# Performance work log

Hardware: AMD Instinct MI355X
Metric: run time of the kernel (lower is better)

Reference implementation:

```python
import jax, jax.numpy as jnp
import numpy as np
import math

B, H, W, C = 8, 32, 32, 512
NUM_HEAD_CHANNELS = 64
NUM_HEADS = C // NUM_HEAD_CHANNELS  # 8
HEAD_DIM = C // NUM_HEADS            # 64
NUM_GROUPS = max(1, C // 16)         # 32
EPS = 1e-6  # flax GroupNorm default epsilon


def setup_inputs() -> dict:
    key = jax.random.key(0)
    ks = jax.random.split(key, 7)
    s = lambda fan: 1.0 / math.sqrt(fan)
    return {
        "x": jax.random.normal(ks[0], (B, H, W, C), jnp.float32),
        "gn_scale": jnp.ones((C,), jnp.float32),
        "gn_bias": jnp.zeros((C,), jnp.float32),
        "w_qkv": jax.random.normal(ks[1], (C, 3 * C), jnp.float32) * s(C),
        "b_qkv": jnp.zeros((3 * C,), jnp.float32),
        "w_out": jax.random.normal(ks[2], (C, C), jnp.float32) * s(C),
        "b_out": jnp.zeros((C,), jnp.float32),
    }


def _group_norm(x, scale, bias):
    # x: (B,H,W,C); normalize per (batch, group) over spatial + in-group channels
    b, h, w, c = x.shape
    xg = x.reshape(b, h * w, NUM_GROUPS, c // NUM_GROUPS)
    mu = jnp.mean(xg, axis=(1, 3), keepdims=True)
    var = jnp.var(xg, axis=(1, 3), keepdims=True)
    xn = (xg - mu) * jax.lax.rsqrt(var + EPS)
    return xn.reshape(b, h, w, c) * scale + bias


def reference(x, gn_scale, gn_bias, w_qkv, b_qkv, w_out, b_out):
    b, h, w, c = x.shape
    seq = h * w
    x_flat = x.reshape(b, seq, c)
    x_norm = _group_norm(x, gn_scale, gn_bias).reshape(b, seq, c)
    qkv = x_norm @ w_qkv + b_qkv                      # (b, seq, 3c)
    q, k, v = jnp.split(qkv, 3, axis=-1)
    scale = 1.0 / math.sqrt(HEAD_DIM)

    def to_heads(t):
        return t.reshape(b, seq, NUM_HEADS, HEAD_DIM).transpose(0, 2, 1, 3)

    q, k, v = to_heads(q), to_heads(k), to_heads(v)
    # NOTE: scale applied to both q and k, matching the original module
    weight = jnp.einsum('bhld,bhsd->bhls', q * scale, k * scale)
    weight = jax.nn.softmax(weight, axis=-1)
    out = jnp.einsum('bhls,bhsd->bhld', weight, v)
    out = out.transpose(0, 2, 1, 3).reshape(b, seq, c)
    out = out @ w_out + b_out
    return (x_flat + out).reshape(b, h, w, c)
```

## Files before the change

kernel.cpp:

```cpp
#include <hip/hip_runtime.h>
#include <hip/hip_bf16.h>

#define SEQ   1024
#define CH    512
#define NHEAD 8
#define HDIM  64
#define BATCH 8

using short8  = __attribute__((ext_vector_type(8))) short;
using short4v = __attribute__((ext_vector_type(4))) short;
using floatx4 = __attribute__((ext_vector_type(4))) float;

__device__ inline unsigned short f2bf(float f) {
  __hip_bfloat16 h = __float2bfloat16(f);
  return __builtin_bit_cast(unsigned short, h);
}

__device__ inline void load_lds16(const void* g, void* l) {
  __builtin_amdgcn_global_load_lds(
      (const __attribute__((address_space(1))) unsigned int*)g,
      (__attribute__((address_space(3))) unsigned int*)l, 16, 0, 0);
}

__global__ __launch_bounds__(256) void prep_stats_kernel(
    const float* __restrict__ wqkv, const float* __restrict__ wout,
    const float* __restrict__ x,
    unsigned short* __restrict__ wqkvt, unsigned short* __restrict__ woutt,
    float2* __restrict__ stats) {
  __shared__ float SH[32 * 33 + 8];
  const int blk = blockIdx.x, tid = threadIdx.x;

  if (blk >= 2048) {
    const float* src; unsigned short* dst; int C, bx, by;
    if (blk < 2816) { int t = blk - 2048; src = wqkv; dst = wqkvt; C = 1536; bx = t % 48; by = t / 48; }
    else { int t = blk - 2816; src = wout; dst = woutt; C = 512; bx = t & 15; by = t >> 4; }
    float (*T)[33] = (float(*)[33])SH;
    int tx = tid & 31, ty = tid >> 5;
    for (int j = 0; j < 4; ++j)
      T[ty + j * 8][tx] = src[(size_t)(by * 32 + ty + j * 8) * C + bx * 32 + tx];
    __syncthreads();
    for (int j = 0; j < 4; ++j)
      dst[(size_t)(bx * 32 + ty + j * 8) * 512 + by * 32 + tx] = f2bf(T[tx][ty + j * 8]);
    return;
  }

  const int bg = blk >> 3, chunk = blk & 7;
  const int b = bg >> 5, g = bg & 31;
  const size_t base = (size_t)b * SEQ * CH + (size_t)chunk * 128 * CH + g * 16;

  float s = 0.f, sq = 0.f;
  for (int i = 0; i < 2; ++i) {
    int c = i * 256 + tid;
    int r = c >> 2, c4 = (c & 3) * 4;
    float4 v = *(const float4*)(x + base + (size_t)r * CH + c4);
    s  += v.x + v.y + v.z + v.w;
    sq += v.x * v.x + v.y * v.y + v.z * v.z + v.w * v.w;
  }
  for (int off = 1; off < 64; off <<= 1) {
    s  += __shfl_xor(s, off);
    sq += __shfl_xor(sq, off);
  }
  float* ls = SH + 1056;
  float* lq = SH + 1060;
  int wid = tid >> 6, lane = tid & 63;
  if (lane == 0) { ls[wid] = s; lq[wid] = sq; }
  __syncthreads();
  if (tid == 0) {
    float2 p;
    p.x = ls[0] + ls[1] + ls[2] + ls[3];
    p.y = lq[0] + lq[1] + lq[2] + lq[3];
    stats[(bg << 3) + chunk] = p;
  }
}

__global__ __launch_bounds__(256) void prep_apply_kernel(
    const float* __restrict__ x, const float* __restrict__ gsc,
    const float* __restrict__ gbs, const float2* __restrict__ stats,
    unsigned short* __restrict__ xn) {
  const int blk = blockIdx.x, tid = threadIdx.x;
  const int bg = blk >> 3, chunk = blk & 7;
  const int b = bg >> 5, g = bg & 31;

  float ts = 0.f, tq = 0.f;
  for (int i = 0; i < 8; ++i) {
    float2 p = stats[(bg << 3) + i];
    ts += p.x; tq += p.y;
  }
  const float inv_n = 1.0f / 16384.0f;
  float mean = ts * inv_n;
  float var  = tq * inv_n - mean * mean;
  float rstd = rsqrtf(var + 1e-6f);

  const size_t base = (size_t)b * SEQ * CH + (size_t)chunk * 128 * CH + g * 16;
  const size_t obase = (size_t)(b * SEQ + chunk * 128) * CH + g * 16;
  int c4 = (tid & 3) * 4;
  float4 sc = *(const float4*)(gsc + g * 16 + c4);
  float4 bs = *(const float4*)(gbs + g * 16 + c4);
  for (int i = 0; i < 2; ++i) {
    int c = i * 256 + tid;
    int r = c >> 2;
    float4 v = *(const float4*)(x + base + (size_t)r * CH + c4);
    ushort4 o;
    o.x = f2bf((v.x - mean) * rstd * sc.x + bs.x);
    o.y = f2bf((v.y - mean) * rstd * sc.y + bs.y);
    o.z = f2bf((v.z - mean) * rstd * sc.z + bs.z);
    o.w = f2bf((v.w - mean) * rstd * sc.w + bs.w);
    *(ushort4*)(xn + obase + (size_t)r * CH + c4) = o;
  }
}

template <int EPI, int MTILE>
__global__ __launch_bounds__(256) void gemm_bt_kernel(
    const unsigned short* __restrict__ A, const unsigned short* __restrict__ Bt,
    int K, int N,
    const float* __restrict__ bias, const float* __restrict__ resid,
    float* __restrict__ outf,
    unsigned short* __restrict__ qb, unsigned short* __restrict__ kb,
    unsigned short* __restrict__ vtb) {
  constexpr int SMSZ = (MTILE == 128) ? 17408 : 16896;
  constexpr int NI   = (MTILE == 128) ? 4 : 2;
  __shared__ alignas(16) unsigned short SM[SMSZ];
  unsigned short* LA = SM;
  unsigned short* LB = SM + MTILE * 64;

  const int tid = threadIdx.x;
  const int wid = tid >> 6, lane = tid & 63;
  const int quad = lane >> 4, m16 = lane & 15;
  const int sw = m16 & 7;
  const int wm = (MTILE == 128) ? (wid & 1) * 64 : 0;
  const int wn = (MTILE == 128) ? (wid >> 1) * 64 : wid * 32;
  const int m0 = blockIdx.x * MTILE, n0 = blockIdx.y * 128;

  floatx4 acc[4][NI];
  for (int i = 0; i < 4; ++i)
    for (int j = 0; j < NI; ++j) acc[i][j] = 0.f;

  for (int k0 = 0; k0 < K; k0 += 64) {
    for (int i = 0; i < MTILE / 32; ++i) {
      int c = i * 256 + tid;
      int r = c >> 3, kc = c & 7;
      load_lds16(A + (size_t)(m0 + r) * K + k0 + ((kc ^ (r & 7)) << 3), &LA[c << 3]);
    }
    for (int i = 0; i < 4; ++i) {
      int c = i * 256 + tid;
      int r = c >> 3, kc = c & 7;
      load_lds16(Bt + (size_t)(n0 + r) * K + k0 + ((kc ^ (r & 7)) << 3), &LB[c << 3]);
    }
    __syncthreads();
    for (int kq = 0; kq < 2; ++kq) {
      int csw = (((kq << 2) + quad) ^ sw) << 3;
      short8 af[4], bf[NI];
      for (int mi = 0; mi < 4; ++mi)
        af[mi] = *(const short8*)&LA[(wm + mi * 16 + m16) * 64 + csw];
      for (int ni = 0; ni < NI; ++ni)
        bf[ni] = *(const short8*)&LB[(wn + ni * 16 + m16) * 64 + csw];
      for (int mi = 0; mi < 4; ++mi)
        for (int ni = 0; ni < NI; ++ni)
          acc[mi][ni] = __builtin_amdgcn_mfma_f32_16x16x32_bf16(af[mi], bf[ni], acc[mi][ni], 0, 0, 0);
    }
    __syncthreads();
  }

  const int b = m0 >> 10;
  if (EPI == 0) {
    const int part = n0 >> 9;
    if (part < 2) {
      const float qscale = (part == 0) ? 0.0225421381f : 1.0f;
      unsigned short* dst = (part == 0) ? qb : kb;
      for (int mi = 0; mi < 4; ++mi)
        for (int ni = 0; ni < 4; ++ni) {
          int ln = wn + ni * 16 + m16;
          float bb = bias[n0 + ln];
          for (int reg = 0; reg < 4; ++reg)
            SM[(wm + mi * 16 + quad * 4 + reg) * 136 + ln] =
                f2bf((acc[mi][ni][reg] + bb) * qscale);
        }
      __syncthreads();
      const int colb = n0 & 511;
      for (int j = 0; j < 8; ++j) {
        int c = j * 256 + tid;
        int m = c >> 4, n8 = (c & 15) * 8;
        int h = (colb + n8) >> 6, d = n8 & 63;
        int sp = (m0 & 1023) + m;
        int4 v = *(const int4*)&SM[m * 136 + n8];
        *(int4*)(dst + (((size_t)(b * NHEAD + h)) * SEQ + sp) * HDIM + d) = v;
      }
    } else {
      for (int mi = 0; mi < 4; ++mi)
        for (int ni = 0; ni < 4; ++ni) {
          int ln = wn + ni * 16 + m16;
          float bb = bias[n0 + ln];
          int mblk = (wm >> 4) + mi;
          int sbase = 32 * (mblk >> 1) + 8 * quad + 4 * (mblk & 1);
          for (int reg = 0; reg < 4; ++reg)
            SM[ln * 136 + sbase + reg] = f2bf(acc[mi][ni][reg] + bb);
        }
      __syncthreads();
      int hbase = (n0 - 1024) >> 6;
      for (int j = 0; j < 8; ++j) {
        int c = j * 256 + tid;
        int ld = c >> 4, sp8 = (c & 15) * 8;
        int h = hbase + (ld >> 6), d = ld & 63;
        int4 v = *(const int4*)&SM[ld * 136 + sp8];
        *(int4*)(vtb + ((size_t)(b * NHEAD + h) * HDIM + d) * SEQ + (m0 & 1023) + sp8) = v;
      }
    }
  } else {
    float* SMf = (float*)SM;
    for (int mi = 0; mi < 4; ++mi)
      for (int ni = 0; ni < NI; ++ni) {
        int ln = wn + ni * 16 + m16;
        float bb = bias[n0 + ln];
        for (int reg = 0; reg < 4; ++reg)
          SMf[(mi * 16 + quad * 4 + reg) * 132 + ln] = acc[mi][ni][reg] + bb;
      }
    __syncthreads();
    for (int j = 0; j < 8; ++j) {
      int c = j * 256 + tid;
      int m = c >> 5, n4 = (c & 31) * 4;
      size_t idx = (size_t)(m0 + m) * N + n0 + n4;
      float4 v = *(const float4*)&SMf[m * 132 + n4];
      float4 rr = *(const float4*)&resid[idx];
      v.x += rr.x; v.y += rr.y; v.z += rr.z; v.w += rr.w;
      *(float4*)&outf[idx] = v;
    }
  }
}

__global__ __launch_bounds__(512) void attn_kernel(
    const unsigned short* __restrict__ qb, const unsigned short* __restrict__ kb,
    const unsigned short* __restrict__ vtb, unsigned short* __restrict__ ao) {
  const int head = blockIdx.x, qt = blockIdx.y;
  const int b = head >> 3, h = head & 7;
  const int tid = threadIdx.x;
  const int wid = tid >> 6, lane = tid & 63;
  const int quad = lane >> 4, m16 = lane & 15;
  const int sw = m16 & 7;

  __shared__ alignas(16) unsigned short sK[8192];
  __shared__ alignas(16) unsigned short sV[8192];

  const unsigned short* kbase = kb  + (size_t)head * SEQ * HDIM;
  const unsigned short* vbase = vtb + (size_t)head * HDIM * SEQ;

  const size_t qrow = (size_t)head * SEQ + qt * 128 + wid * 16 + m16;
  short8 aq0 = *(const short8*)(qb + qrow * HDIM + quad * 8);
  short8 aq1 = *(const short8*)(qb + qrow * HDIM + 32 + quad * 8);

  float lacc = 0.f;
  floatx4 o[4];
  for (int df = 0; df < 4; ++df) o[df] = 0.f;

  for (int kt = 0; kt < 8; ++kt) {
    for (int i = 0; i < 2; ++i) {
      int c = i * 512 + tid;
      int r = c >> 3, kc = c & 7;
      load_lds16(kbase + (kt * 128 + r) * HDIM + ((kc ^ (r & 7)) << 3), &sK[c << 3]);
    }
    for (int i = 0; i < 2; ++i) {
      int c = i * 512 + tid;
      int d = c >> 4, kc = c & 15;
      load_lds16(vbase + d * SEQ + kt * 128 + ((kc ^ (d & 7)) << 3), &sV[c << 3]);
    }
    __syncthreads();

    short8 pf32[4];
    for (int sf = 0; sf < 8; ++sf) {
      const int rb = (sf * 16 + m16) * 64;
      short8 k0 = *(const short8*)&sK[rb + ((quad ^ sw) << 3)];
      short8 k1 = *(const short8*)&sK[rb + (((4 + quad) ^ sw) << 3)];
      floatx4 s = 0.f;
      s = __builtin_amdgcn_mfma_f32_16x16x32_bf16(k0, aq0, s, 0, 0, 0);
      s = __builtin_amdgcn_mfma_f32_16x16x32_bf16(k1, aq1, s, 0, 0, 0);
      const int u = sf >> 1, t4 = (sf & 1) * 4;
      for (int r = 0; r < 4; ++r) {
        float p = exp2f(s[r]);
        lacc += p;
        pf32[u][t4 + r] = (short)f2bf(p);
      }
    }

    for (int u = 0; u < 4; ++u) {
      const int chunk = ((u * 4 + quad) ^ sw) << 3;
      for (int df = 0; df < 4; ++df) {
        short8 bv = *(const short8*)&sV[(df * 16 + m16) * 128 + chunk];
        o[df] = __builtin_amdgcn_mfma_f32_16x16x32_bf16(pf32[u], bv, o[df], 0, 0, 0);
      }
    }
    __syncthreads();
  }

  lacc += __shfl_xor(lacc, 16);
  lacc += __shfl_xor(lacc, 32);
  lacc = 1.0f / lacc;
  float l0 = __shfl(lacc, quad * 4 + 0);
  float l1 = __shfl(lacc, quad * 4 + 1);
  float l2 = __shfl(lacc, quad * 4 + 2);
  float l3 = __shfl(lacc, quad * 4 + 3);
  int qg = qt * 128 + wid * 16 + quad * 4;
  for (int df = 0; df < 4; ++df) {
    int col = h * HDIM + df * 16 + m16;
    size_t base = (size_t)(b * SEQ + qg) * CH + col;
    ao[base + 0 * CH] = f2bf(o[df][0] * l0);
    ao[base + 1 * CH] = f2bf(o[df][1] * l1);
    ao[base + 2 * CH] = f2bf(o[df][2] * l2);
    ao[base + 3 * CH] = f2bf(o[df][3] * l3);
  }
}

extern "C" void kernel_launch(void* const* d_in, const int* in_sizes, int n_in,
                              void* d_out, int out_size, void* d_ws, size_t ws_size,
                              hipStream_t stream) {
  const float* x    = (const float*)d_in[0];
  const float* gsc  = (const float*)d_in[1];
  const float* gbs  = (const float*)d_in[2];
  const float* wqkv = (const float*)d_in[3];
  const float* bqkv = (const float*)d_in[4];
  const float* wout = (const float*)d_in[5];
  const float* bout = (const float*)d_in[6];
  float* out = (float*)d_out;

  char* ws = (char*)d_ws;
  unsigned short* xn    = (unsigned short*)(ws);
  unsigned short* wqkvt = (unsigned short*)(ws + 8388608);
  unsigned short* woutt = (unsigned short*)(ws + 9961472);
  unsigned short* qb    = (unsigned short*)(ws + 10485760);
  unsigned short* kb    = (unsigned short*)(ws + 18874368);
  unsigned short* vtb   = (unsigned short*)(ws + 27262976);
  unsigned short* ao    = (unsigned short*)(ws + 35651584);
  float2*         stats = (float2*)(ws + 44040192);

  prep_stats_kernel<<<3072, 256, 0, stream>>>(wqkv, wout, x, wqkvt, woutt, stats);
  prep_apply_kernel<<<2048, 256, 0, stream>>>(x, gsc, gbs, stats, xn);
  gemm_bt_kernel<0, 128><<<dim3(64, 12), 256, 0, stream>>>(
      xn, wqkvt, 512, 1536, bqkv, nullptr, nullptr, qb, kb, vtb);
  attn_kernel<<<dim3(64, 8), 512, 0, stream>>>(qb, kb, vtb, ao);
  gemm_bt_kernel<1, 64><<<dim3(128, 4), 256, 0, stream>>>(
      ao, woutt, 512, 512, bout, x, out, nullptr, nullptr, nullptr);
}
```

Measured before the change: 150.2 us.

## Rewrite attention with 32x32x16 MFMA, double-buffered padded LDS tiles, larger query tiles

The attention kernel moves from 16x16x32 MFMA to 32x32x16 MFMA. Each block now covers 256 queries, each wave 32, and keys stream in 64-wide tiles through double-buffered, padded LDS (row stride 72) in place of XOR swizzling. The next tile is prefetched while the current one is computed, and the V-transpose layout in the QKV GEMM epilogue is changed to match the new operand ordering. This halves the number of attention blocks and raises per-wave MFMA efficiency, but the fewer, larger blocks may reduce occupancy.

```diff
diff --git a/kernel.cpp b/kernel.cpp
--- a/kernel.cpp
+++ b/kernel.cpp
@@ -7,9 +7,9 @@
 #define HDIM  64
 #define BATCH 8
 
-using short8  = __attribute__((ext_vector_type(8))) short;
-using short4v = __attribute__((ext_vector_type(4))) short;
-using floatx4 = __attribute__((ext_vector_type(4))) float;
+using short8   = __attribute__((ext_vector_type(8))) short;
+using floatx4  = __attribute__((ext_vector_type(4))) float;
+using floatx16 = __attribute__((ext_vector_type(16))) float;
 
 __device__ inline unsigned short f2bf(float f) {
   __hip_bfloat16 h = __float2bfloat16(f);
@@ -92,7 +92,6 @@
   float rstd = rsqrtf(var + 1e-6f);
 
   const size_t base = (size_t)b * SEQ * CH + (size_t)chunk * 128 * CH + g * 16;
-  const size_t obase = (size_t)(b * SEQ + chunk * 128) * CH + g * 16;
   int c4 = (tid & 3) * 4;
   float4 sc = *(const float4*)(gsc + g * 16 + c4);
   float4 bs = *(const float4*)(gbs + g * 16 + c4);
@@ -105,7 +104,7 @@
     o.y = f2bf((v.y - mean) * rstd * sc.y + bs.y);
     o.z = f2bf((v.z - mean) * rstd * sc.z + bs.z);
     o.w = f2bf((v.w - mean) * rstd * sc.w + bs.w);
-    *(ushort4*)(xn + obase + (size_t)r * CH + c4) = o;
+    *(ushort4*)(xn + base + (size_t)r * CH + c4) = o;
   }
 }
 
@@ -186,12 +185,12 @@
         *(int4*)(dst + (((size_t)(b * NHEAD + h)) * SEQ + sp) * HDIM + d) = v;
       }
     } else {
+      const int qswap = ((quad & 1) << 1) | (quad >> 1);
       for (int mi = 0; mi < 4; ++mi)
         for (int ni = 0; ni < 4; ++ni) {
           int ln = wn + ni * 16 + m16;
           float bb = bias[n0 + ln];
-          int mblk = (wm >> 4) + mi;
-          int sbase = 32 * (mblk >> 1) + 8 * quad + 4 * (mblk & 1);
+          int sbase = wm + mi * 16 + qswap * 4;
           for (int reg = 0; reg < 4; ++reg)
             SM[ln * 136 + sbase + reg] = f2bf(acc[mi][ni][reg] + bb);
         }
@@ -234,78 +233,85 @@
   const int b = head >> 3, h = head & 7;
   const int tid = threadIdx.x;
   const int wid = tid >> 6, lane = tid & 63;
-  const int quad = lane >> 4, m16 = lane & 15;
-  const int sw = m16 & 7;
-
-  __shared__ alignas(16) unsigned short sK[8192];
-  __shared__ alignas(16) unsigned short sV[8192];
+  const int l31 = lane & 31, half = lane >> 5;
+
+  __shared__ alignas(16) unsigned short sK[2][64 * 72];
+  __shared__ alignas(16) unsigned short sV[2][64 * 72];
 
   const unsigned short* kbase = kb  + (size_t)head * SEQ * HDIM;
   const unsigned short* vbase = vtb + (size_t)head * HDIM * SEQ;
 
-  const size_t qrow = (size_t)head * SEQ + qt * 128 + wid * 16 + m16;
-  short8 aq0 = *(const short8*)(qb + qrow * HDIM + quad * 8);
-  short8 aq1 = *(const short8*)(qb + qrow * HDIM + 32 + quad * 8);
+  auto stage = [&](int kt, int bf) {
+    {
+      int c = tid;
+      int r = c / 9, kc = c - r * 9;
+      int col = (kc == 8) ? 0 : kc;
+      load_lds16(kbase + (size_t)(kt * 64 + r) * HDIM + col * 8, &sK[bf][c * 8]);
+      load_lds16(vbase + (size_t)r * SEQ + kt * 64 + col * 8, &sV[bf][c * 8]);
+    }
+    if (tid < 64) {
+      int c = 512 + tid;
+      int r = c / 9, kc = c - r * 9;
+      int col = (kc == 8) ? 0 : kc;
+      load_lds16(kbase + (size_t)(kt * 64 + r) * HDIM + col * 8, &sK[bf][c * 8]);
+      load_lds16(vbase + (size_t)r * SEQ + kt * 64 + col * 8, &sV[bf][c * 8]);
+    }
+  };
+
+  const size_t qrow = (size_t)head * SEQ + qt * 256 + wid * 32 + l31;
+  short8 qf[4];
+  for (int dstep = 0; dstep < 4; ++dstep)
+    qf[dstep] = *(const short8*)(qb + qrow * HDIM + dstep * 16 + half * 8);
 
   float lacc = 0.f;
-  floatx4 o[4];
-  for (int df = 0; df < 4; ++df) o[df] = 0.f;
-
-  for (int kt = 0; kt < 8; ++kt) {
-    for (int i = 0; i < 2; ++i) {
-      int c = i * 512 + tid;
-      int r = c >> 3, kc = c & 7;
-      load_lds16(kbase + (kt * 128 + r) * HDIM + ((kc ^ (r & 7)) << 3), &sK[c << 3]);
-    }
-    for (int i = 0; i < 2; ++i) {
-      int c = i * 512 + tid;
-      int d = c >> 4, kc = c & 15;
-      load_lds16(vbase + d * SEQ + kt * 128 + ((kc ^ (d & 7)) << 3), &sV[c << 3]);
-    }
-    __syncthreads();
-
-    short8 pf32[4];
-    for (int sf = 0; sf < 8; ++sf) {
-      const int rb = (sf * 16 + m16) * 64;
-      short8 k0 = *(const short8*)&sK[rb + ((quad ^ sw) << 3)];
-      short8 k1 = *(const short8*)&sK[rb + (((4 + quad) ^ sw) << 3)];
-      floatx4 s = 0.f;
-      s = __builtin_amdgcn_mfma_f32_16x16x32_bf16(k0, aq0, s, 0, 0, 0);
-      s = __builtin_amdgcn_mfma_f32_16x16x32_bf16(k1, aq1, s, 0, 0, 0);
-      const int u = sf >> 1, t4 = (sf & 1) * 4;
-      for (int r = 0; r < 4; ++r) {
-        float p = exp2f(s[r]);
-        lacc += p;
-        pf32[u][t4 + r] = (short)f2bf(p);
+  floatx16 o0 = 0.f, o1 = 0.f;
+
+  stage(0, 0);
+  for (int kt = 0; kt < 16; ++kt) {
+    const int bf = kt & 1;
+    __syncthreads();
+    if (kt < 15) stage(kt + 1, bf ^ 1);
+
+    for (int sf = 0; sf < 2; ++sf) {
+      floatx16 st = 0.f;
+      const unsigned short* kr = &sK[bf][(sf * 32 + l31) * 72 + half * 8];
+      for (int dstep = 0; dstep < 4; ++dstep)
+        st = __builtin_amdgcn_mfma_f32_32x32x16_bf16(
+            *(const short8*)(kr + dstep * 16), qf[dstep], st, 0, 0, 0);
+
+      short8 pf0, pf1;
+      for (int j = 0; j < 8; ++j) {
+        float p0 = exp2f(st[j]);
+        float p1 = exp2f(st[8 + j]);
+        lacc += p0 + p1;
+        pf0[j] = (short)f2bf(p0);
+        pf1[j] = (short)f2bf(p1);
       }
-    }
-
-    for (int u = 0; u < 4; ++u) {
-      const int chunk = ((u * 4 + quad) ^ sw) << 3;
-      for (int df = 0; df < 4; ++df) {
-        short8 bv = *(const short8*)&sV[(df * 16 + m16) * 128 + chunk];
-        o[df] = __builtin_amdgcn_mfma_f32_16x16x32_bf16(pf32[u], bv, o[df], 0, 0, 0);
-      }
-    }
-    __syncthreads();
-  }
-
-  lacc += __shfl_xor(lacc, 16);
+
+      const unsigned short* vr0 = &sV[bf][l31 * 72];
+      const unsigned short* vr1 = &sV[bf][(32 + l31) * 72];
+      int c0 = (sf * 4 + half) * 8;
+      int c1 = (sf * 4 + 2 + half) * 8;
+      o0 = __builtin_amdgcn_mfma_f32_32x32x16_bf16(pf0, *(const short8*)(vr0 + c0), o0, 0, 0, 0);
+      o1 = __builtin_amdgcn_mfma_f32_32x32x16_bf16(pf0, *(const short8*)(vr1 + c0), o1, 0, 0, 0);
+      o0 = __builtin_amdgcn_mfma_f32_32x32x16_bf16(pf1, *(const short8*)(vr0 + c1), o0, 0, 0, 0);
+      o1 = __builtin_amdgcn_mfma_f32_32x32x16_bf16(pf1, *(const short8*)(vr1 + c1), o1, 0, 0, 0);
+    }
+  }
+
   lacc += __shfl_xor(lacc, 32);
-  lacc = 1.0f / lacc;
-  float l0 = __shfl(lacc, quad * 4 + 0);
-  float l1 = __shfl(lacc, quad * 4 + 1);
-  float l2 = __shfl(lacc, quad * 4 + 2);
-  float l3 = __shfl(lacc, quad * 4 + 3);
-  int qg = qt * 128 + wid * 16 + quad * 4;
-  for (int df = 0; df < 4; ++df) {
-    int col = h * HDIM + df * 16 + m16;
-    size_t base = (size_t)(b * SEQ + qg) * CH + col;
-    ao[base + 0 * CH] = f2bf(o[df][0] * l0);
-    ao[base + 1 * CH] = f2bf(o[df][1] * l1);
-    ao[base + 2 * CH] = f2bf(o[df][2] * l2);
-    ao[base + 3 * CH] = f2bf(o[df][3] * l3);
-  }
+  float linv = 1.0f / lacc;
+
+  const int qg0 = qt * 256 + wid * 32;
+  for (int pr = 0; pr < 4; ++pr)
+    for (int i = 0; i < 4; ++i) {
+      int reg = pr * 4 + i;
+      int ql = i + half * 4 + pr * 8;
+      float lr = __shfl(linv, ql);
+      size_t base = (size_t)(b * SEQ + qg0 + ql) * CH + h * HDIM;
+      ao[base + l31]      = f2bf(o0[reg] * lr);
+      ao[base + 32 + l31] = f2bf(o1[reg] * lr);
+    }
 }
 
 extern "C" void kernel_launch(void* const* d_in, const int* in_sizes, int n_in,
@@ -334,7 +340,7 @@
   prep_apply_kernel<<<2048, 256, 0, stream>>>(x, gsc, gbs, stats, xn);
   gemm_bt_kernel<0, 128><<<dim3(64, 12), 256, 0, stream>>>(
       xn, wqkvt, 512, 1536, bqkv, nullptr, nullptr, qb, kb, vtb);
-  attn_kernel<<<dim3(64, 8), 512, 0, stream>>>(qb, kb, vtb, ao);
+  attn_kernel<<<dim3(64, 4), 512, 0, stream>>>(qb, kb, vtb, ao);
   gemm_bt_kernel<1, 64><<<dim3(128, 4), 256, 0, stream>>>(
       ao, woutt, 512, 512, bout, x, out, nullptr, nullptr, nullptr);
 }
```

New measurement: 156.6 us. 4.3% more time.
